# Optimization experiments

Measured on AMD Instinct MI355X. Metric: run time of the kernel, lower is better.

The kernel has to match this reference:

```python
import jax, jax.numpy as jnp
import numpy as np

N = 262144
K = 4  # Kernel_Correlation k
EPS = 1e-5


def setup_inputs() -> dict:
    key = jax.random.key(0)
    ks = jax.random.split(key, 12)
    inp = {
        "corner": jax.random.normal(ks[0], (N, 9), jnp.float32),
        "normal": jax.random.normal(ks[1], (N, 3), jnp.float32),
        "neighbour": jax.random.randint(ks[2], (N, 3), 0, N, jnp.int64),
        # Conv1d(1,32,6) on a length-6 signal == linear [32,6] (+bias)
        "conv_w": jax.random.normal(ks[3], (32, 6), jnp.float32) * 0.2,
        "conv_b": jax.random.normal(ks[4], (32,), jnp.float32) * 0.1,
        "lin3_w": jax.random.normal(ks[5], (64, 32), jnp.float32) * 0.15,
        "lin3_b": jnp.zeros((64,), jnp.float32),
        "lin4_w": jax.random.normal(ks[6], (64, 64), jnp.float32) * 0.12,
        "lin4_b": jnp.zeros((64,), jnp.float32),
        "kernel": jax.random.normal(ks[7], (64, K, 3), jnp.float32),  # learnable RBF kernel
        # 1x1 Conv1d(131,131) == linear [131,131]
        "conv1_w": jax.random.normal(ks[8], (131, 131), jnp.float32) * 0.08,
        "conv1_b": jnp.zeros((131,), jnp.float32),
        "bn_g": jnp.ones((131,), jnp.float32),
        "bn_b": jnp.zeros((131,), jnp.float32),
        "conv2_w": jax.random.normal(ks[9], (131, 131), jnp.float32) * 0.08,
        "conv2_b": jnp.zeros((131,), jnp.float32),
    }
    return inp


def reference(corner, normal, neighbour, conv_w, conv_b, lin3_w, lin3_b,
              lin4_w, lin4_b, kernel, conv1_w, conv1_b, bn_g, bn_b,
              conv2_w, conv2_b):
    # ---- Face_Rotate_Conv (vectorized over all n faces) ----
    c1, c2, c3 = corner[:, 0:3], corner[:, 3:6], corner[:, 6:9]
    # three rotated corner pairs: [n, 3, 6]
    pairs = jnp.stack([jnp.concatenate([c1, c2], 1),
                       jnp.concatenate([c2, c3], 1),
                       jnp.concatenate([c3, c1], 1)], axis=1)
    conv = jnp.einsum('npd,od->npo', pairs, conv_w) + conv_b  # [n,3,32]
    v = conv.mean(axis=1)                                      # [n,32]
    v = jax.nn.relu(v @ lin3_w.T + lin3_b) @ lin4_w.T + lin4_b  # [n,64]

    # ---- Kernel_Correlation (neighbour indices are gathered but unused
    # in the original math; only normal_i enters the RBF) ----
    # ||n_i - kernel_{m,l}||^2 via expansion; sq: [n,64,K]
    sq = (jnp.sum(normal * normal, 1)[:, None, None]
          + jnp.sum(kernel * kernel, -1)[None]
          - 2.0 * jnp.einsum('nd,mld->nml', normal, kernel))
    # original: sum_l exp(-norm^2) / (2*sigma^2), sigma=1, then / (k*4)
    z = jnp.sum(jnp.exp(-sq), axis=-1) * (0.5 / (K * 4))       # [n,64]

    # ---- structural_Des head ----
    x = jnp.concatenate([normal, v, z], axis=1)                # [n,131]
    h = x @ conv1_w.T + conv1_b
    # BatchNorm1d(131) in training mode: stats over the n dim (L=1)
    mean = h.mean(axis=0)
    var = jnp.mean((h - mean) ** 2, axis=0)
    h = bn_g * (h - mean) * jax.lax.rsqrt(var + EPS) + bn_b
    h = jax.nn.relu(h)
    out = h @ conv2_w.T + conv2_b                              # [n,131]
    return out
```

## Files before the change

kernel.cpp:

```cpp
#include <hip/hip_runtime.h>

#define NROWS 262144
#define PLANE_B   8388608ull
#define PLANE_US  4194304ull
#define KS 168

#define H_B    0ull
#define W1P_B  75497472ull
#define W2P_B  75545856ull
#define B1P_B  75594240ull
#define G4_B   75594816ull
#define ZT_B   75595840ull
#define SUMS_B 75599936ull

typedef short  short8 __attribute__((ext_vector_type(8)));
typedef float  f32x4  __attribute__((ext_vector_type(4)));

static __device__ __forceinline__ unsigned short f2bf(float f) {
    unsigned u = __float_as_uint(f);
    u = u + 0x7fffu + ((u >> 16) & 1u);
    return (unsigned short)(u >> 16);
}
static __device__ __forceinline__ float bf2f(unsigned short h) {
    return __uint_as_float(((unsigned)h) << 16);
}

__global__ __launch_bounds__(64) void k_prep(
    const float* __restrict__ conv_w, const float* __restrict__ conv_b,
    const float* __restrict__ lin3_w, const float* __restrict__ lin3_b,
    const float* __restrict__ lin4_w, const float* __restrict__ lin4_b,
    const float* __restrict__ kern,
    const float* __restrict__ w1, const float* __restrict__ b1,
    const float* __restrict__ w2,
    unsigned short* __restrict__ W1P, unsigned short* __restrict__ W2P,
    float* __restrict__ B1P, float* __restrict__ G4, float* __restrict__ ZT)
{
    const int j = blockIdx.x;
    const int l = threadIdx.x;
    if (j < 144) {
        const bool jv = (j < 131);
        float acc = 0.0f;
        if (jv) {
            #pragma unroll 4
            for (int o = 0; o < 64; o++)
                acc += w1[j * 131 + 3 + o] * lin4_w[o * 64 + l];
        }
        W1P[j * KS + l]      = jv ? f2bf(acc) : (unsigned short)0;
        W1P[j * KS + 64 + l] = jv ? f2bf(w1[j * 131 + 67 + l]) : (unsigned short)0;
        if (l < 40) {
            float v = (jv && l < 3) ? w1[j * 131 + l] : 0.0f;
            W1P[j * KS + 128 + l] = f2bf(v);
        }
        W2P[j * KS + l]      = jv ? f2bf(w2[j * 131 + l]) : (unsigned short)0;
        W2P[j * KS + 64 + l] = (jv && (64 + l) < 131) ? f2bf(w2[j * 131 + 64 + l]) : (unsigned short)0;
        if (l < 40) {
            int k2 = 128 + l;
            W2P[j * KS + k2] = (jv && k2 < 131) ? f2bf(w2[j * 131 + k2]) : (unsigned short)0;
        }
        if (l == 0) {
            float bb = 0.0f;
            if (jv) {
                bb = b1[j];
                for (int o = 0; o < 64; o++) bb += w1[j * 131 + 3 + o] * lin4_b[o];
            }
            B1P[j] = bb;
        }
    } else if (j == 144) {
        float g0v = lin3_b[l], ga = 0.0f, gb = 0.0f, gc = 0.0f;
        #pragma unroll 4
        for (int i = 0; i < 32; i++) {
            float wv = lin3_w[l * 32 + i];
            ga  += wv * (conv_w[i * 6 + 0] + conv_w[i * 6 + 3]);
            gb  += wv * (conv_w[i * 6 + 1] + conv_w[i * 6 + 4]);
            gc  += wv * (conv_w[i * 6 + 2] + conv_w[i * 6 + 5]);
            g0v += wv * conv_b[i];
        }
        G4[l * 4 + 0] = ga; G4[l * 4 + 1] = gb; G4[l * 4 + 2] = gc; G4[l * 4 + 3] = g0v;
    } else {
        #pragma unroll
        for (int p = 0; p < 4; p++) {
            int idx = l * 4 + p;
            float kx = kern[idx * 3 + 0], ky = kern[idx * 3 + 1], kz = kern[idx * 3 + 2];
            ZT[idx * 4 + 0] = 2.0f * kx;
            ZT[idx * 4 + 1] = 2.0f * ky;
            ZT[idx * 4 + 2] = 2.0f * kz;
            ZT[idx * 4 + 3] = -(kx * kx + ky * ky + kz * kz);
        }
    }
}

__global__ __launch_bounds__(128) void k_F(
    const float* __restrict__ corner, const float* __restrict__ normal,
    const unsigned short* __restrict__ W1P, const float* __restrict__ B1P,
    const float* __restrict__ G4, const float* __restrict__ ZT,
    unsigned short* __restrict__ H, float* __restrict__ sums)
{
    __shared__ unsigned short Xs[128 * KS];
    __shared__ unsigned short mini[2 * 64 * 20];
    __shared__ float sl[288];

    const int tid  = threadIdx.x;
    const int wave = tid >> 6, lane = tid & 63;
    const int kg   = lane >> 4, c15 = lane & 15;
    const int row  = blockIdx.x * 128 + tid;

    for (int i = tid; i < 288; i += 128) sl[i] = 0.0f;

    const float* cp = corner + (size_t)row * 9;
    float c0 = cp[0], c1 = cp[1], c2 = cp[2], c3 = cp[3], c4 = cp[4],
          c5 = cp[5], c6 = cp[6], c7 = cp[7], c8 = cp[8];
    const float n0 = normal[row * 3 + 0];
    const float n1 = normal[row * 3 + 1];
    const float n2 = normal[row * 3 + 2];
    const float m0 = (c0 + c3 + c6) * (1.0f / 3.0f);
    const float m1 = (c1 + c4 + c7) * (1.0f / 3.0f);
    const float m2 = (c2 + c5 + c8) * (1.0f / 3.0f);
    const float nn = n0 * n0 + n1 * n1 + n2 * n2;

    unsigned short* xrow = Xs + tid * KS;

    #pragma unroll
    for (int q = 0; q < 8; q++) {
        short8 pk;
        #pragma unroll
        for (int e = 0; e < 8; e++) {
            int o = q * 8 + e;
            float u = G4[o * 4 + 3] + m0 * G4[o * 4 + 0] + m1 * G4[o * 4 + 1] + m2 * G4[o * 4 + 2];
            pk[e] = (short)f2bf(fmaxf(u, 0.0f));
        }
        *(short8*)(xrow + q * 8) = pk;
    }
    #pragma unroll
    for (int q = 0; q < 8; q++) {
        short8 pk;
        #pragma unroll
        for (int e = 0; e < 8; e++) {
            int mi = q * 8 + e;
            float acc = 0.0f;
            #pragma unroll
            for (int lp = 0; lp < 4; lp++) {
                const float* zt = ZT + (mi * 4 + lp) * 4;
                float w = zt[3] + zt[0] * n0 + zt[1] * n1 + zt[2] * n2 - nn;
                acc += __expf(w);
            }
            pk[e] = (short)f2bf(acc * 0.03125f);
        }
        *(short8*)(xrow + 64 + q * 8) = pk;
    }
    {
        short8 pk = {0, 0, 0, 0, 0, 0, 0, 0};
        pk[0] = (short)f2bf(n0); pk[1] = (short)f2bf(n1); pk[2] = (short)f2bf(n2);
        *(short8*)(xrow + 128) = pk;
        short8 zz = {0, 0, 0, 0, 0, 0, 0, 0};
        *(short8*)(xrow + 136) = zz;
        *(short8*)(xrow + 144) = zz;
        *(short8*)(xrow + 152) = zz;
    }

    __syncthreads();

    short8 af[4][5];
    #pragma unroll
    for (int mi = 0; mi < 4; mi++)
        #pragma unroll
        for (int ks = 0; ks < 5; ks++)
            af[mi][ks] = *(const short8*)(Xs + (wave * 64 + mi * 16 + c15) * KS + ks * 32 + kg * 8);

    #pragma unroll 1
    for (int n = 0; n < 9; n++) {
        const int col = n * 16 + c15;
        const float bias = B1P[col];
        short8 bf[5];
        #pragma unroll
        for (int ks = 0; ks < 5; ks++)
            bf[ks] = *(const short8*)(W1P + (size_t)col * KS + ks * 32 + kg * 8);
        float s1 = 0.0f, s2 = 0.0f;
        #pragma unroll
        for (int mi = 0; mi < 4; mi++) {
            f32x4 acc = {bias, bias, bias, bias};
            #pragma unroll
            for (int ks = 0; ks < 5; ks++)
                acc = __builtin_amdgcn_mfma_f32_16x16x32_bf16(af[mi][ks], bf[ks], acc, 0, 0, 0);
            #pragma unroll
            for (int r = 0; r < 4; r++) {
                s1 += acc[r]; s2 += acc[r] * acc[r];
                mini[(wave * 64 + mi * 16 + kg * 4 + r) * 20 + c15] = f2bf(acc[r]);
            }
        }
        s1 += __shfl_xor(s1, 16); s2 += __shfl_xor(s2, 16);
        s1 += __shfl_xor(s1, 32); s2 += __shfl_xor(s2, 32);
        if (lane < 16) { atomicAdd(&sl[col], s1); atomicAdd(&sl[144 + col], s2); }
        asm volatile("s_waitcnt lgkmcnt(0)" ::: "memory");
        __builtin_amdgcn_sched_barrier(0);
        const uint2* q = (const uint2*)(mini + (wave * 64 + lane) * 20);
        uint2 q0 = q[0], q1 = q[1], q2 = q[2], q3 = q[3];
        uint4* dst = (uint4*)((char*)H + (size_t)n * PLANE_B +
                              (size_t)(blockIdx.x * 128 + wave * 64 + lane) * 32);
        dst[0] = make_uint4(q0.x, q0.y, q1.x, q1.y);
        dst[1] = make_uint4(q2.x, q2.y, q3.x, q3.y);
    }

    __syncthreads();
    {
        float* d = sums + (blockIdx.x & 31) * 288;
        for (int i = tid; i < 288; i += 128) atomicAdd(&d[i], sl[i]);
    }
}

__global__ __launch_bounds__(256) void k_B(
    const unsigned short* __restrict__ H, const unsigned short* __restrict__ W2P,
    const float* __restrict__ sums,
    const float* __restrict__ bn_g, const float* __restrict__ bn_b,
    const float* __restrict__ b2, float* __restrict__ out)
{
    __shared__ unsigned short Bs[144 * KS];
    __shared__ __align__(16) float s_scale[160];
    __shared__ __align__(16) float s_shift[160];

    const int tid  = threadIdx.x;
    {
        const uint4* src = (const uint4*)W2P;
        uint4* dst = (uint4*)Bs;
        #pragma unroll
        for (int i = 0; i < 12; i++) {
            int idx = tid + i * 256;
            if (idx < 3024) dst[idx] = src[idx];
        }
    }
    if (tid < 160) {
        float sc = 0.0f, sh = 0.0f;
        if (tid < 131) {
            float s1 = 0.0f, s2 = 0.0f;
            #pragma unroll 4
            for (int s = 0; s < 32; s++) {
                s1 += sums[s * 288 + tid];
                s2 += sums[s * 288 + 144 + tid];
            }
            const float inv = 1.0f / (float)NROWS;
            float mean = s1 * inv;
            float var  = fmaxf(s2 * inv - mean * mean, 0.0f);
            sc = bn_g[tid] * rsqrtf(var + 1e-5f);
            sh = bn_b[tid] - mean * sc;
        }
        s_scale[tid] = sc; s_shift[tid] = sh;
    }
    __syncthreads();

    const int wave = tid >> 6, lane = tid & 63;
    const int kg   = lane >> 4, c15 = lane & 15;
    const int rwave = blockIdx.x * 256 + wave * 64;

    #pragma unroll 1
    for (int mp = 0; mp < 2; mp++) {
        short8 af[2][5];
        #pragma unroll
        for (int mi = 0; mi < 2; mi++) {
            int arow = rwave + mp * 32 + mi * 16 + c15;
            #pragma unroll
            for (int ks = 0; ks < 5; ks++) {
                short8 res = {0, 0, 0, 0, 0, 0, 0, 0};
                if (ks < 4 || kg < 2) {
                    int p = (ks < 4) ? (ks * 2 + (kg >> 1)) : 8;
                    short8 h8 = *(const short8*)(H + (size_t)p * PLANE_US +
                                                 (size_t)arow * 16 + (kg & 1) * 8);
                    int c0 = ks * 32 + kg * 8;
                    #pragma unroll
                    for (int e = 0; e < 8; e++) {
                        float hf = bf2f((unsigned short)h8[e]);
                        res[e] = (short)f2bf(fmaxf(hf * s_scale[c0 + e] + s_shift[c0 + e], 0.0f));
                    }
                }
                af[mi][ks] = res;
            }
        }
        #pragma unroll 1
        for (int n = 0; n < 9; n++) {
            const int col = n * 16 + c15;
            const float bias = (col < 131) ? b2[col] : 0.0f;
            short8 bf[5];
            #pragma unroll
            for (int ks = 0; ks < 5; ks++)
                bf[ks] = *(const short8*)&Bs[(unsigned)col * KS + ks * 32 + kg * 8];
            f32x4 acc0 = {bias, bias, bias, bias};
            f32x4 acc1 = {bias, bias, bias, bias};
            #pragma unroll
            for (int ks = 0; ks < 5; ks++) {
                acc0 = __builtin_amdgcn_mfma_f32_16x16x32_bf16(af[0][ks], bf[ks], acc0, 0, 0, 0);
                acc1 = __builtin_amdgcn_mfma_f32_16x16x32_bf16(af[1][ks], bf[ks], acc1, 0, 0, 0);
            }
            if (col < 131) {
                #pragma unroll
                for (int r = 0; r < 4; r++) {
                    out[(size_t)(rwave + mp * 32 + kg * 4 + r) * 131 + col]      = acc0[r];
                    out[(size_t)(rwave + mp * 32 + 16 + kg * 4 + r) * 131 + col] = acc1[r];
                }
            }
        }
    }
}

extern "C" void kernel_launch(void* const* d_in, const int* in_sizes, int n_in,
                              void* d_out, int out_size, void* d_ws, size_t ws_size,
                              hipStream_t stream) {
    (void)in_sizes; (void)n_in; (void)out_size; (void)ws_size;
    const float* corner = (const float*)d_in[0];
    const float* normal = (const float*)d_in[1];
    const float* conv_w = (const float*)d_in[3];
    const float* conv_b = (const float*)d_in[4];
    const float* lin3_w = (const float*)d_in[5];
    const float* lin3_b = (const float*)d_in[6];
    const float* lin4_w = (const float*)d_in[7];
    const float* lin4_b = (const float*)d_in[8];
    const float* kern   = (const float*)d_in[9];
    const float* w1     = (const float*)d_in[10];
    const float* b1     = (const float*)d_in[11];
    const float* bn_g   = (const float*)d_in[12];
    const float* bn_b   = (const float*)d_in[13];
    const float* w2     = (const float*)d_in[14];
    const float* b2     = (const float*)d_in[15];

    char* wsb = (char*)d_ws;
    unsigned short* Hp  = (unsigned short*)(wsb + H_B);
    unsigned short* W1P = (unsigned short*)(wsb + W1P_B);
    unsigned short* W2P = (unsigned short*)(wsb + W2P_B);
    float* B1P  = (float*)(wsb + B1P_B);
    float* G4   = (float*)(wsb + G4_B);
    float* ZT   = (float*)(wsb + ZT_B);
    float* sums = (float*)(wsb + SUMS_B);
    float* outp = (float*)d_out;

    hipMemsetAsync(sums, 0, 32 * 288 * sizeof(float), stream);
    k_prep<<<146, 64, 0, stream>>>(conv_w, conv_b, lin3_w, lin3_b, lin4_w, lin4_b,
                                   kern, w1, b1, w2, W1P, W2P, B1P, G4, ZT);
    k_F<<<NROWS / 128, 128, 0, stream>>>(corner, normal, W1P, B1P, G4, ZT, Hp, sums);
    k_B<<<NROWS / 256, 256, 0, stream>>>(Hp, W2P, sums, bn_g, bn_b, b2, outp);
}
```

Measured before the change: 315.8 us.

## Build MFMA A-fragments in registers, drop LDS staging, fold memset into prep

Measured after the change: 607.4 us. 1.92x slower.

```diff
diff --git a/kernel.cpp b/kernel.cpp
--- a/kernel.cpp
+++ b/kernel.cpp
@@ -33,7 +33,8 @@
     const float* __restrict__ w1, const float* __restrict__ b1,
     const float* __restrict__ w2,
     unsigned short* __restrict__ W1P, unsigned short* __restrict__ W2P,
-    float* __restrict__ B1P, float* __restrict__ G4, float* __restrict__ ZT)
+    float* __restrict__ B1P, float* __restrict__ G4, float* __restrict__ ZT,
+    float* __restrict__ sums)
 {
     const int j = blockIdx.x;
     const int l = threadIdx.x;
@@ -76,7 +77,7 @@
             g0v += wv * conv_b[i];
         }
         G4[l * 4 + 0] = ga; G4[l * 4 + 1] = gb; G4[l * 4 + 2] = gc; G4[l * 4 + 3] = g0v;
-    } else {
+    } else if (j == 145) {
         #pragma unroll
         for (int p = 0; p < 4; p++) {
             int idx = l * 4 + p;
@@ -86,85 +87,83 @@
             ZT[idx * 4 + 2] = 2.0f * kz;
             ZT[idx * 4 + 3] = -(kx * kx + ky * ky + kz * kz);
         }
-    }
-}
-
-__global__ __launch_bounds__(128) void k_F(
+    } else {
+        #pragma unroll
+        for (int q = 0; q < 144; q++) sums[q * 64 + l] = 0.0f;
+    }
+}
+
+__global__ __launch_bounds__(256, 4) void k_F(
     const float* __restrict__ corner, const float* __restrict__ normal,
     const unsigned short* __restrict__ W1P, const float* __restrict__ B1P,
     const float* __restrict__ G4, const float* __restrict__ ZT,
     unsigned short* __restrict__ H, float* __restrict__ sums)
 {
-    __shared__ unsigned short Xs[128 * KS];
-    __shared__ unsigned short mini[2 * 64 * 20];
+    __shared__ unsigned short mini[4][32][20];
     __shared__ float sl[288];
 
     const int tid  = threadIdx.x;
     const int wave = tid >> 6, lane = tid & 63;
     const int kg   = lane >> 4, c15 = lane & 15;
-    const int row  = blockIdx.x * 128 + tid;
-
-    for (int i = tid; i < 288; i += 128) sl[i] = 0.0f;
-
-    const float* cp = corner + (size_t)row * 9;
-    float c0 = cp[0], c1 = cp[1], c2 = cp[2], c3 = cp[3], c4 = cp[4],
-          c5 = cp[5], c6 = cp[6], c7 = cp[7], c8 = cp[8];
-    const float n0 = normal[row * 3 + 0];
-    const float n1 = normal[row * 3 + 1];
-    const float n2 = normal[row * 3 + 2];
-    const float m0 = (c0 + c3 + c6) * (1.0f / 3.0f);
-    const float m1 = (c1 + c4 + c7) * (1.0f / 3.0f);
-    const float m2 = (c2 + c5 + c8) * (1.0f / 3.0f);
-    const float nn = n0 * n0 + n1 * n1 + n2 * n2;
-
-    unsigned short* xrow = Xs + tid * KS;
-
+    const int rowbase = blockIdx.x * 128 + wave * 32;
+
+    for (int i = tid; i < 288; i += 256) sl[i] = 0.0f;
+    __syncthreads();
+
+    const int r0 = rowbase + c15, r1 = rowbase + 16 + c15;
+    const float* cp0 = corner + (size_t)r0 * 9;
+    const float* cp1 = corner + (size_t)r1 * 9;
+    const float m00 = (cp0[0] + cp0[3] + cp0[6]) * (1.0f / 3.0f);
+    const float m01 = (cp0[1] + cp0[4] + cp0[7]) * (1.0f / 3.0f);
+    const float m02 = (cp0[2] + cp0[5] + cp0[8]) * (1.0f / 3.0f);
+    const float m10 = (cp1[0] + cp1[3] + cp1[6]) * (1.0f / 3.0f);
+    const float m11 = (cp1[1] + cp1[4] + cp1[7]) * (1.0f / 3.0f);
+    const float m12 = (cp1[2] + cp1[5] + cp1[8]) * (1.0f / 3.0f);
+    const float n00 = normal[r0 * 3 + 0], n01 = normal[r0 * 3 + 1], n02 = normal[r0 * 3 + 2];
+    const float n10 = normal[r1 * 3 + 0], n11 = normal[r1 * 3 + 1], n12 = normal[r1 * 3 + 2];
+    const float nn0 = n00 * n00 + n01 * n01 + n02 * n02;
+    const float nn1 = n10 * n10 + n11 * n11 + n12 * n12;
+
+    short8 af[2][5];
     #pragma unroll
-    for (int q = 0; q < 8; q++) {
-        short8 pk;
+    for (int ks = 0; ks < 2; ks++) {
+        short8 p0, p1;
         #pragma unroll
         for (int e = 0; e < 8; e++) {
-            int o = q * 8 + e;
-            float u = G4[o * 4 + 3] + m0 * G4[o * 4 + 0] + m1 * G4[o * 4 + 1] + m2 * G4[o * 4 + 2];
-            pk[e] = (short)f2bf(fmaxf(u, 0.0f));
-        }
-        *(short8*)(xrow + q * 8) = pk;
+            const f32x4 g = *(const f32x4*)(G4 + (ks * 32 + kg * 8 + e) * 4);
+            float u0 = g[3] + m00 * g[0] + m01 * g[1] + m02 * g[2];
+            float u1 = g[3] + m10 * g[0] + m11 * g[1] + m12 * g[2];
+            p0[e] = (short)f2bf(fmaxf(u0, 0.0f));
+            p1[e] = (short)f2bf(fmaxf(u1, 0.0f));
+        }
+        af[0][ks] = p0; af[1][ks] = p1;
     }
     #pragma unroll
-    for (int q = 0; q < 8; q++) {
-        short8 pk;
+    for (int ks = 2; ks < 4; ks++) {
+        short8 p0, p1;
         #pragma unroll
         for (int e = 0; e < 8; e++) {
-            int mi = q * 8 + e;
-            float acc = 0.0f;
+            const int zi = (ks - 2) * 32 + kg * 8 + e;
+            float a0 = 0.0f, a1 = 0.0f;
             #pragma unroll
             for (int lp = 0; lp < 4; lp++) {
-                const float* zt = ZT + (mi * 4 + lp) * 4;
-                float w = zt[3] + zt[0] * n0 + zt[1] * n1 + zt[2] * n2 - nn;
-                acc += __expf(w);
-            }
-            pk[e] = (short)f2bf(acc * 0.03125f);
-        }
-        *(short8*)(xrow + 64 + q * 8) = pk;
+                const f32x4 zt = *(const f32x4*)(ZT + (zi * 4 + lp) * 4);
+                a0 += __expf(zt[3] + zt[0] * n00 + zt[1] * n01 + zt[2] * n02 - nn0);
+                a1 += __expf(zt[3] + zt[0] * n10 + zt[1] * n11 + zt[2] * n12 - nn1);
+            }
+            p0[e] = (short)f2bf(a0 * 0.03125f);
+            p1[e] = (short)f2bf(a1 * 0.03125f);
+        }
+        af[0][ks] = p0; af[1][ks] = p1;
     }
     {
-        short8 pk = {0, 0, 0, 0, 0, 0, 0, 0};
-        pk[0] = (short)f2bf(n0); pk[1] = (short)f2bf(n1); pk[2] = (short)f2bf(n2);
-        *(short8*)(xrow + 128) = pk;
-        short8 zz = {0, 0, 0, 0, 0, 0, 0, 0};
-        *(short8*)(xrow + 136) = zz;
-        *(short8*)(xrow + 144) = zz;
-        *(short8*)(xrow + 152) = zz;
-    }
-
-    __syncthreads();
-
-    short8 af[4][5];
-    #pragma unroll
-    for (int mi = 0; mi < 4; mi++)
-        #pragma unroll
-        for (int ks = 0; ks < 5; ks++)
-            af[mi][ks] = *(const short8*)(Xs + (wave * 64 + mi * 16 + c15) * KS + ks * 32 + kg * 8);
+        short8 p0 = {0,0,0,0,0,0,0,0}, p1 = {0,0,0,0,0,0,0,0};
+        if (kg == 0) {
+            p0[0] = (short)f2bf(n00); p0[1] = (short)f2bf(n01); p0[2] = (short)f2bf(n02);
+            p1[0] = (short)f2bf(n10); p1[1] = (short)f2bf(n11); p1[2] = (short)f2bf(n12);
+        }
+        af[0][4] = p0; af[1][4] = p1;
+    }
 
     #pragma unroll 1
     for (int n = 0; n < 9; n++) {
@@ -174,59 +173,51 @@
         #pragma unroll
         for (int ks = 0; ks < 5; ks++)
             bf[ks] = *(const short8*)(W1P + (size_t)col * KS + ks * 32 + kg * 8);
-        float s1 = 0.0f, s2 = 0.0f;
-        #pragma unroll
-        for (int mi = 0; mi < 4; mi++) {
-            f32x4 acc = {bias, bias, bias, bias};
-            #pragma unroll
-            for (int ks = 0; ks < 5; ks++)
-                acc = __builtin_amdgcn_mfma_f32_16x16x32_bf16(af[mi][ks], bf[ks], acc, 0, 0, 0);
-            #pragma unroll
-            for (int r = 0; r < 4; r++) {
-                s1 += acc[r]; s2 += acc[r] * acc[r];
-                mini[(wave * 64 + mi * 16 + kg * 4 + r) * 20 + c15] = f2bf(acc[r]);
-            }
-        }
+        f32x4 acc0 = {bias, bias, bias, bias};
+        f32x4 acc1 = {bias, bias, bias, bias};
+        #pragma unroll
+        for (int ks = 0; ks < 5; ks++) {
+            acc0 = __builtin_amdgcn_mfma_f32_16x16x32_bf16(af[0][ks], bf[ks], acc0, 0, 0, 0);
+            acc1 = __builtin_amdgcn_mfma_f32_16x16x32_bf16(af[1][ks], bf[ks], acc1, 0, 0, 0);
+        }
+        float s1 = acc0[0] + acc0[1] + acc0[2] + acc0[3]
+                 + acc1[0] + acc1[1] + acc1[2] + acc1[3];
+        float s2 = acc0[0]*acc0[0] + acc0[1]*acc0[1] + acc0[2]*acc0[2] + acc0[3]*acc0[3]
+                 + acc1[0]*acc1[0] + acc1[1]*acc1[1] + acc1[2]*acc1[2] + acc1[3]*acc1[3];
         s1 += __shfl_xor(s1, 16); s2 += __shfl_xor(s2, 16);
         s1 += __shfl_xor(s1, 32); s2 += __shfl_xor(s2, 32);
         if (lane < 16) { atomicAdd(&sl[col], s1); atomicAdd(&sl[144 + col], s2); }
+        #pragma unroll
+        for (int r = 0; r < 4; r++) {
+            mini[wave][kg * 4 + r][c15]      = f2bf(acc0[r]);
+            mini[wave][16 + kg * 4 + r][c15] = f2bf(acc1[r]);
+        }
         asm volatile("s_waitcnt lgkmcnt(0)" ::: "memory");
         __builtin_amdgcn_sched_barrier(0);
-        const uint2* q = (const uint2*)(mini + (wave * 64 + lane) * 20);
-        uint2 q0 = q[0], q1 = q[1], q2 = q[2], q3 = q[3];
-        uint4* dst = (uint4*)((char*)H + (size_t)n * PLANE_B +
-                              (size_t)(blockIdx.x * 128 + wave * 64 + lane) * 32);
-        dst[0] = make_uint4(q0.x, q0.y, q1.x, q1.y);
-        dst[1] = make_uint4(q2.x, q2.y, q3.x, q3.y);
+        const int rr = lane >> 1, hh = lane & 1;
+        const uint2* q = (const uint2*)&mini[wave][rr][hh * 8];
+        uint2 q0 = q[0], q1 = q[1];
+        *(uint4*)((char*)H + (size_t)n * PLANE_B + (size_t)(rowbase + rr) * 32 + hh * 16)
+            = make_uint4(q0.x, q0.y, q1.x, q1.y);
     }
 
     __syncthreads();
     {
         float* d = sums + (blockIdx.x & 31) * 288;
-        for (int i = tid; i < 288; i += 128) atomicAdd(&d[i], sl[i]);
-    }
-}
-
-__global__ __launch_bounds__(256) void k_B(
+        for (int i = tid; i < 288; i += 256) atomicAdd(&d[i], sl[i]);
+    }
+}
+
+__global__ __launch_bounds__(256, 4) void k_B(
     const unsigned short* __restrict__ H, const unsigned short* __restrict__ W2P,
     const float* __restrict__ sums,
     const float* __restrict__ bn_g, const float* __restrict__ bn_b,
     const float* __restrict__ b2, float* __restrict__ out)
 {
-    __shared__ unsigned short Bs[144 * KS];
     __shared__ __align__(16) float s_scale[160];
     __shared__ __align__(16) float s_shift[160];
 
-    const int tid  = threadIdx.x;
-    {
-        const uint4* src = (const uint4*)W2P;
-        uint4* dst = (uint4*)Bs;
-        #pragma unroll
-        for (int i = 0; i < 12; i++) {
-            int idx = tid + i * 256;
-            if (idx < 3024) dst[idx] = src[idx];
-        }
-    }
+    const int tid = threadIdx.x;
     if (tid < 160) {
         float sc = 0.0f, sh = 0.0f;
         if (tid < 131) {
@@ -280,7 +271,7 @@
             short8 bf[5];
             #pragma unroll
             for (int ks = 0; ks < 5; ks++)
-                bf[ks] = *(const short8*)&Bs[(unsigned)col * KS + ks * 32 + kg * 8];
+                bf[ks] = *(const short8*)(W2P + (size_t)col * KS + ks * 32 + kg * 8);
             f32x4 acc0 = {bias, bias, bias, bias};
             f32x4 acc1 = {bias, bias, bias, bias};
             #pragma unroll
@@ -329,9 +320,8 @@
     float* sums = (float*)(wsb + SUMS_B);
     float* outp = (float*)d_out;
 
-    hipMemsetAsync(sums, 0, 32 * 288 * sizeof(float), stream);
-    k_prep<<<146, 64, 0, stream>>>(conv_w, conv_b, lin3_w, lin3_b, lin4_w, lin4_b,
-                                   kern, w1, b1, w2, W1P, W2P, B1P, G4, ZT);
-    k_F<<<NROWS / 128, 128, 0, stream>>>(corner, normal, W1P, B1P, G4, ZT, Hp, sums);
+    k_prep<<<147, 64, 0, stream>>>(conv_w, conv_b, lin3_w, lin3_b, lin4_w, lin4_b,
+                                   kern, w1, b1, w2, W1P, W2P, B1P, G4, ZT, sums);
+    k_F<<<NROWS / 128, 256, 0, stream>>>(corner, normal, W1P, B1P, G4, ZT, Hp, sums);
     k_B<<<NROWS / 256, 256, 0, stream>>>(Hp, W2P, sums, bn_g, bn_b, b2, outp);
 }
```
